# Kernel tuning notes

Measured on AMD Instinct MI355X. Metric: run time of the kernel, lower is better.

The kernel has to match this reference:

```python
import jax, jax.numpy as jnp
import numpy as np

B = 2048
NUM_FIELDS = 32
EMBED = 64
P = NUM_FIELDS * (NUM_FIELDS - 1) // 2  # 496 field pairs

# Pair indices (i < j), identical to the row_idx/col_idx loops in __init__
_ROW, _COL = np.triu_indices(NUM_FIELDS, k=1)
ROW_IDX = jnp.asarray(_ROW, dtype=jnp.int32)
COL_IDX = jnp.asarray(_COL, dtype=jnp.int32)


def setup_inputs() -> dict:
    key = jax.random.key(0)
    k1, k2 = jax.random.split(key)
    emb_inputs = jax.random.normal(k1, (B, NUM_FIELDS, EMBED), dtype=jnp.float32)
    # kernel_type='mat' -> kernel shape (E, P, E), xavier_normal-like init
    fan_in = P * EMBED
    fan_out = EMBED
    std = float(np.sqrt(2.0 / (fan_in + fan_out)))
    kernel = jax.random.normal(k2, (EMBED, P, EMBED), dtype=jnp.float32) * std
    return {"emb_inputs": emb_inputs, "kernel": kernel}


def reference(emb_inputs, kernel):
    # Gather field pairs: p, q shape (B, P, E)
    p = emb_inputs[:, ROW_IDX]
    q = emb_inputs[:, COL_IDX]
    # torch named-tensor chain for kernel_type='mat':
    #   kp[b, h, n] = sum_e p[b, n, e] * kernel[h, n, e]
    #   out[b, n]   = sum_h kp[b, h, n] * q[b, n, h]
    # Fused: out[b, n] = sum_{e, h} p[b, n, e] * kernel[h, n, e] * q[b, n, h]
    return jnp.einsum('bne,hne,bnh->bn', p, kernel, q)
```

## Files before the change

kernel.cpp:

```cpp
#include <hip/hip_runtime.h>


#define B_TOT 2048
#define NF    32
#define EMB   64
#define NP    496
#define BT    64

typedef short bf16x8 __attribute__((ext_vector_type(8)));
typedef short bf16x4 __attribute__((ext_vector_type(4)));
typedef float f32x4  __attribute__((ext_vector_type(4)));
typedef float f32x16 __attribute__((ext_vector_type(16)));

static __device__ inline unsigned f2bf(float f) {
    unsigned u = __builtin_bit_cast(unsigned, f);
    u += 0x7fffu + ((u >> 16) & 1u);
    return u >> 16;
}
static __device__ inline unsigned pack2(float lo, float hi) {
    return f2bf(lo) | (f2bf(hi) << 16);
}
static __device__ inline float bf2f(short s) {
    return __builtin_bit_cast(float, (unsigned)((unsigned short)s) << 16);
}

#define AS1 __attribute__((address_space(1)))
#define AS3 __attribute__((address_space(3)))

__device__ const unsigned char PAIR_T16[120] = {
    0x01,0x02,0x03,0x04,0x05,0x06,0x07,0x08,0x09,0x0A,0x0B,0x0C,0x0D,0x0E,0x0F,
    0x12,0x13,0x14,0x15,0x16,0x17,0x18,0x19,0x1A,0x1B,0x1C,0x1D,0x1E,0x1F,
    0x23,0x24,0x25,0x26,0x27,0x28,0x29,0x2A,0x2B,0x2C,0x2D,0x2E,0x2F,
    0x34,0x35,0x36,0x37,0x38,0x39,0x3A,0x3B,0x3C,0x3D,0x3E,0x3F,
    0x45,0x46,0x47,0x48,0x49,0x4A,0x4B,0x4C,0x4D,0x4E,0x4F,
    0x56,0x57,0x58,0x59,0x5A,0x5B,0x5C,0x5D,0x5E,0x5F,
    0x67,0x68,0x69,0x6A,0x6B,0x6C,0x6D,0x6E,0x6F,
    0x78,0x79,0x7A,0x7B,0x7C,0x7D,0x7E,0x7F,
    0x89,0x8A,0x8B,0x8C,0x8D,0x8E,0x8F,
    0x9A,0x9B,0x9C,0x9D,0x9E,0x9F,
    0xAB,0xAC,0xAD,0xAE,0xAF,
    0xBC,0xBD,0xBE,0xBF,
    0xCD,0xCE,0xCF,
    0xDE,0xDF,
    0xEF
};

__global__ __launch_bounds__(256) void prep(const float* __restrict__ kern,
                                            const float* __restrict__ emb,
                                            short* __restrict__ kb,
                                            short* __restrict__ ebf) {
    __shared__ short w[EMB * 72];
    if (blockIdx.x < NP) {
        const int n = blockIdx.x;
#pragma unroll
        for (int j = 0; j < 4; ++j) {
            const int idx = threadIdx.x + 256 * j;
            const int h = idx >> 4, e4 = idx & 15;
            const f32x4 v = *(const f32x4*)(kern + ((size_t)h * NP + n) * EMB + e4 * 4);
            uint2 u;
            u.x = pack2(v[0], v[1]);
            u.y = pack2(v[2], v[3]);
            *(uint2*)&w[h * 72 + e4 * 4] = u;
        }
        __syncthreads();
#pragma unroll
        for (int j = 0; j < 2; ++j) {
            const int u    = threadIdx.x + 256 * j;
            const int frag = u >> 6, l = u & 63;
            const int h  = (frag >> 2) * 32 + (l & 31);
            const int e0 = (frag & 3) * 16 + (l >> 5) * 8;
            const bf16x8 t = *(const bf16x8*)&w[h * 72 + e0];
            *(bf16x8*)(kb + (size_t)n * 4096 + u * 8) = t;
        }
    } else {
        const int t    = (blockIdx.x - NP) * 256 + threadIdx.x;
        const int cidx = t & 127;
        const int f    = (t >> 7) & 31;
        const int bt16 = t >> 12;
        const int bp = cidx >> 3, x = cidx & 7;
        const int ec = x ^ (bp & 7);
        const float* src = emb + (((size_t)(bt16 * 16 + bp) * NF + f) * EMB + ec * 8);
        const f32x4 a = *(const f32x4*)src;
        const f32x4 b = *(const f32x4*)(src + 4);
        uint4 u;
        u.x = pack2(a[0], a[1]); u.y = pack2(a[2], a[3]);
        u.z = pack2(b[0], b[1]); u.w = pack2(b[2], b[3]);
        *(uint4*)(ebf + (size_t)t * 8) = u;
    }
}

__global__ __launch_bounds__(1024) void opnl_main(
    const short* __restrict__ ebf,
    const short* __restrict__ kb,
    float* __restrict__ out)
{
    __shared__ short elds[64 * 1024];

    const int type = blockIdx.x >> 5;
    const int bt   = blockIdx.x & 31;
    const int b0   = bt * BT;

    int bLo, bHi, npr;
    switch (type) {
        case 0: case 1: bLo = 0;  bHi = 0;  npr = 60; break;
        case 2: case 3: bLo = 16; bHi = 16; npr = 60; break;
        case 4:         bLo = 0;  bHi = 8;  npr = 64; break;
        case 5:         bLo = 8;  bHi = 16; npr = 64; break;
        case 6:         bLo = 0;  bHi = 16; npr = 64; break;
        default:        bLo = 8;  bHi = 8;  npr = 64; break;
    }

    const int lane = threadIdx.x & 63;
    const int wid  = threadIdx.x >> 6;
    const int bp   = lane & 15;
    const int l5   = lane >> 5;
    const int sub_lo = (lane >> 4) & 1;

#pragma unroll
    for (int i = 0; i < 4; ++i) {
        const int s     = wid * 4 + i;
        const int lf    = s >> 2, sub16 = s & 3;
        const int gf    = lf + (lf < 8 ? bLo : bHi);
        const short* src = ebf + ((size_t)((bt * 4 + sub16) * 32 + gf)) * 1024;
        __builtin_amdgcn_global_load_lds((const AS1 void*)(src + lane * 8),
                                         (AS3 void*)&elds[s * 1024], 16, 0, 0);
        __builtin_amdgcn_global_load_lds((const AS1 void*)(src + 512 + lane * 8),
                                         (AS3 void*)&elds[s * 1024 + 512], 16, 0, 0);
    }
    __syncthreads();

    for (int k = 0; k < 4; ++k) {
        int pr = wid + 16 * k;
        if (pr >= npr) pr -= npr;
        int lr, lc;
        if (type < 4) {
            const int pig = __builtin_amdgcn_readfirstlane((type & 1) * 60 + pr);
            const int byt = PAIR_T16[pig];
            lr = byt >> 4; lc = byt & 15;
        } else {
            lr = pr >> 3; lc = 8 + (pr & 7);
        }
        const int R  = lr + (lr < 8 ? bLo : bHi);
        const int C  = lc + (lc < 8 ? bLo : bHi);
        const int nn = R * (63 - R) / 2 + (C - R - 1);

        bf16x8 wf[2][4];
        const bf16x8* wp = (const bf16x8*)(kb + (size_t)nn * 4096);
#pragma unroll
        for (int mt = 0; mt < 2; ++mt)
#pragma unroll
            for (int ks = 0; ks < 4; ++ks)
                wf[mt][ks] = wp[(mt * 4 + ks) * 64 + lane];

#pragma unroll
        for (int hb = 0; hb < 2; ++hb) {
            const int sub16 = hb * 2 + sub_lo;
            const int segp  = (lr * 4 + sub16) * 1024;
            const int segq  = (lc * 4 + sub16) * 1024;

            bf16x8 pf[4];
#pragma unroll
            for (int ks = 0; ks < 4; ++ks) {
                const int ec = ks * 2 + l5;
                pf[ks] = *(const bf16x8*)&elds[segp + (bp * 8 + (ec ^ (bp & 7))) * 8];
            }

            f32x16 acc[2] = {
                f32x16{0,0,0,0,0,0,0,0,0,0,0,0,0,0,0,0},
                f32x16{0,0,0,0,0,0,0,0,0,0,0,0,0,0,0,0}};
#pragma unroll
            for (int ks = 0; ks < 4; ++ks) {
                acc[0] = __builtin_amdgcn_mfma_f32_32x32x16_bf16(
                    wf[0][ks], pf[ks], acc[0], 0, 0, 0);
                acc[1] = __builtin_amdgcn_mfma_f32_32x32x16_bf16(
                    wf[1][ks], pf[ks], acc[1], 0, 0, 0);
            }

            float val = 0.f;
#pragma unroll
            for (int mt = 0; mt < 2; ++mt) {
#pragma unroll
                for (int rg2 = 0; rg2 < 4; ++rg2) {
                    const bf16x4 qv = *(const bf16x4*)
                        &elds[segq + (bp * 8 + ((mt * 4 + rg2) ^ (bp & 7))) * 8 + l5 * 4];
#pragma unroll
                    for (int i = 0; i < 4; ++i)
                        val = fmaf(acc[mt][rg2 * 4 + i], bf2f(qv[i]), val);
                }
            }
            val += __shfl_xor(val, 32, 64);
            if (lane < 32) out[(size_t)(b0 + hb * 32 + lane) * NP + nn] = val;
        }
    }
}

extern "C" void kernel_launch(void* const* d_in, const int* in_sizes, int n_in,
                              void* d_out, int out_size, void* d_ws, size_t ws_size,
                              hipStream_t stream) {
    const float* emb  = (const float*)d_in[0];
    const float* kern = (const float*)d_in[1];
    float*       out  = (float*)d_out;

    short* kb  = (short*)d_ws;
    short* ebf = (short*)((char*)d_ws + (4 << 20));

    prep<<<NP + (B_TOT * NF * EMB / 8) / 256, 256, 0, stream>>>(kern, emb, kb, ebf);
    opnl_main<<<8 * 32, 1024, 0, stream>>>(ebf, kb, out);
}
```

Baseline: 29.31 us.

## Fuse prep and main kernels into one cooperative launch with grid sync

Merges the bf16 conversion/relayout prep kernel and the MFMA main kernel into a single cooperative kernel of 256 blocks that first converts embeddings and kernel weights, then synchronizes the whole grid before computing. It is meant to remove the second kernel launch and the inter-kernel gap. In exchange it pays for a grid-wide barrier, runs the prep phase with only 256 blocks of 1024 threads, and requires all 256 blocks to be co-resident.

```diff
diff --git a/kernel.cpp b/kernel.cpp
--- a/kernel.cpp
+++ b/kernel.cpp
@@ -1,4 +1,7 @@
 #include <hip/hip_runtime.h>
+#include <hip/hip_cooperative_groups.h>
+
+namespace cg = cooperative_groups;
 
 
 #define B_TOT 2048
@@ -45,35 +48,20 @@
     0xEF
 };
 
-__global__ __launch_bounds__(256) void prep(const float* __restrict__ kern,
-                                            const float* __restrict__ emb,
-                                            short* __restrict__ kb,
-                                            short* __restrict__ ebf) {
-    __shared__ short w[EMB * 72];
-    if (blockIdx.x < NP) {
-        const int n = blockIdx.x;
-#pragma unroll
-        for (int j = 0; j < 4; ++j) {
-            const int idx = threadIdx.x + 256 * j;
-            const int h = idx >> 4, e4 = idx & 15;
-            const f32x4 v = *(const f32x4*)(kern + ((size_t)h * NP + n) * EMB + e4 * 4);
-            uint2 u;
-            u.x = pack2(v[0], v[1]);
-            u.y = pack2(v[2], v[3]);
-            *(uint2*)&w[h * 72 + e4 * 4] = u;
-        }
-        __syncthreads();
-#pragma unroll
-        for (int j = 0; j < 2; ++j) {
-            const int u    = threadIdx.x + 256 * j;
-            const int frag = u >> 6, l = u & 63;
-            const int h  = (frag >> 2) * 32 + (l & 31);
-            const int e0 = (frag & 3) * 16 + (l >> 5) * 8;
-            const bf16x8 t = *(const bf16x8*)&w[h * 72 + e0];
-            *(bf16x8*)(kb + (size_t)n * 4096 + u * 8) = t;
-        }
-    } else {
-        const int t    = (blockIdx.x - NP) * 256 + threadIdx.x;
+__global__ __launch_bounds__(1024) void opnl_fused(
+    const float* __restrict__ emb,
+    const float* __restrict__ kern,
+    short* __restrict__ kb,
+    short* __restrict__ ebf,
+    float* __restrict__ out)
+{
+    __shared__ short elds[64 * 1024];
+
+    const int tid = threadIdx.x;
+
+#pragma unroll
+    for (int jt = 0; jt < 2; ++jt) {
+        const int t    = blockIdx.x * 1024 + tid + jt * (256 * 1024);
         const int cidx = t & 127;
         const int f    = (t >> 7) & 31;
         const int bt16 = t >> 12;
@@ -87,14 +75,31 @@
         u.z = pack2(b[0], b[1]); u.w = pack2(b[2], b[3]);
         *(uint4*)(ebf + (size_t)t * 8) = u;
     }
-}
-
-__global__ __launch_bounds__(1024) void opnl_main(
-    const short* __restrict__ ebf,
-    const short* __restrict__ kb,
-    float* __restrict__ out)
-{
-    __shared__ short elds[64 * 1024];
+
+    if (blockIdx.x < 248) {
+#pragma unroll
+        for (int jn = 0; jn < 2; ++jn) {
+            const int n  = blockIdx.x * 2 + jn;
+            const int h  = tid >> 4, e4 = tid & 15;
+            const f32x4 v = *(const f32x4*)(kern + ((size_t)h * NP + n) * EMB + e4 * 4);
+            uint2 u;
+            u.x = pack2(v[0], v[1]);
+            u.y = pack2(v[2], v[3]);
+            *(uint2*)&elds[jn * 4608 + h * 72 + e4 * 4] = u;
+        }
+        __syncthreads();
+        {
+            const int jn = tid >> 9, u = tid & 511;
+            const int n  = blockIdx.x * 2 + jn;
+            const int frag = u >> 6, l = u & 63;
+            const int h  = (frag >> 2) * 32 + (l & 31);
+            const int e0 = (frag & 3) * 16 + (l >> 5) * 8;
+            const bf16x8 t = *(const bf16x8*)&elds[jn * 4608 + h * 72 + e0];
+            *(bf16x8*)(kb + (size_t)n * 4096 + u * 8) = t;
+        }
+    }
+
+    cg::this_grid().sync();
 
     const int type = blockIdx.x >> 5;
     const int bt   = blockIdx.x & 31;
@@ -110,8 +115,8 @@
         default:        bLo = 8;  bHi = 8;  npr = 64; break;
     }
 
-    const int lane = threadIdx.x & 63;
-    const int wid  = threadIdx.x >> 6;
+    const int lane = tid & 63;
+    const int wid  = tid >> 6;
     const int bp   = lane & 15;
     const int l5   = lane >> 5;
     const int sub_lo = (lane >> 4) & 1;
@@ -204,6 +209,7 @@
     short* kb  = (short*)d_ws;
     short* ebf = (short*)((char*)d_ws + (4 << 20));
 
-    prep<<<NP + (B_TOT * NF * EMB / 8) / 256, 256, 0, stream>>>(kern, emb, kb, ebf);
-    opnl_main<<<8 * 32, 1024, 0, stream>>>(ebf, kb, out);
-}
+    void* args[] = {(void*)&emb, (void*)&kern, (void*)&kb, (void*)&ebf, (void*)&out};
+    hipLaunchCooperativeKernel((void*)opnl_fused, dim3(256), dim3(1024),
+                               args, 0, stream);
+}
```

New measurement: 76.67 us. +161.6%, slower.

## Fuse embedding bf16 conversion into main kernel, drop intermediate buffer

Applied to the files above, without the earlier changes.

The prep kernel no longer converts embeddings to a swizzled bf16 workspace buffer. The main kernel now reads fp32 embeddings directly from global memory, converts them to bf16 in registers and writes them into the swizzled LDS layout. Block index mapping also changes to interleave the eight pair types within each batch tile, which may improve L2 reuse of the embedding rows. This removes a global write and re-read of the bf16 embedding copy, but each main block now reads twice as many bytes (fp32) and does conversion work before the barrier. Embedding rows are also re-read from global by all eight type blocks.

```diff
diff --git a/kernel.cpp b/kernel.cpp
--- a/kernel.cpp
+++ b/kernel.cpp
@@ -23,9 +23,6 @@
 static __device__ inline float bf2f(short s) {
     return __builtin_bit_cast(float, (unsigned)((unsigned short)s) << 16);
 }
-
-#define AS1 __attribute__((address_space(1)))
-#define AS3 __attribute__((address_space(3)))
 
 __device__ const unsigned char PAIR_T16[120] = {
     0x01,0x02,0x03,0x04,0x05,0x06,0x07,0x08,0x09,0x0A,0x0B,0x0C,0x0D,0x0E,0x0F,
@@ -45,59 +42,41 @@
     0xEF
 };
 
-__global__ __launch_bounds__(256) void prep(const float* __restrict__ kern,
-                                            const float* __restrict__ emb,
-                                            short* __restrict__ kb,
-                                            short* __restrict__ ebf) {
+__global__ __launch_bounds__(256) void prep_kern(const float* __restrict__ kern,
+                                                 short* __restrict__ kb) {
+    const int n = blockIdx.x;
     __shared__ short w[EMB * 72];
-    if (blockIdx.x < NP) {
-        const int n = blockIdx.x;
-#pragma unroll
-        for (int j = 0; j < 4; ++j) {
-            const int idx = threadIdx.x + 256 * j;
-            const int h = idx >> 4, e4 = idx & 15;
-            const f32x4 v = *(const f32x4*)(kern + ((size_t)h * NP + n) * EMB + e4 * 4);
-            uint2 u;
-            u.x = pack2(v[0], v[1]);
-            u.y = pack2(v[2], v[3]);
-            *(uint2*)&w[h * 72 + e4 * 4] = u;
-        }
-        __syncthreads();
-#pragma unroll
-        for (int j = 0; j < 2; ++j) {
-            const int u    = threadIdx.x + 256 * j;
-            const int frag = u >> 6, l = u & 63;
-            const int h  = (frag >> 2) * 32 + (l & 31);
-            const int e0 = (frag & 3) * 16 + (l >> 5) * 8;
-            const bf16x8 t = *(const bf16x8*)&w[h * 72 + e0];
-            *(bf16x8*)(kb + (size_t)n * 4096 + u * 8) = t;
-        }
-    } else {
-        const int t    = (blockIdx.x - NP) * 256 + threadIdx.x;
-        const int cidx = t & 127;
-        const int f    = (t >> 7) & 31;
-        const int bt16 = t >> 12;
-        const int bp = cidx >> 3, x = cidx & 7;
-        const int ec = x ^ (bp & 7);
-        const float* src = emb + (((size_t)(bt16 * 16 + bp) * NF + f) * EMB + ec * 8);
-        const f32x4 a = *(const f32x4*)src;
-        const f32x4 b = *(const f32x4*)(src + 4);
-        uint4 u;
-        u.x = pack2(a[0], a[1]); u.y = pack2(a[2], a[3]);
-        u.z = pack2(b[0], b[1]); u.w = pack2(b[2], b[3]);
-        *(uint4*)(ebf + (size_t)t * 8) = u;
+#pragma unroll
+    for (int j = 0; j < 4; ++j) {
+        const int idx = threadIdx.x + 256 * j;
+        const int h = idx >> 4, e4 = idx & 15;
+        const f32x4 v = *(const f32x4*)(kern + ((size_t)h * NP + n) * EMB + e4 * 4);
+        uint2 u;
+        u.x = pack2(v[0], v[1]);
+        u.y = pack2(v[2], v[3]);
+        *(uint2*)&w[h * 72 + e4 * 4] = u;
+    }
+    __syncthreads();
+#pragma unroll
+    for (int j = 0; j < 2; ++j) {
+        const int u    = threadIdx.x + 256 * j;
+        const int frag = u >> 6, l = u & 63;
+        const int h  = (frag >> 2) * 32 + (l & 31);
+        const int e0 = (frag & 3) * 16 + (l >> 5) * 8;
+        const bf16x8 t = *(const bf16x8*)&w[h * 72 + e0];
+        *(bf16x8*)(kb + (size_t)n * 4096 + u * 8) = t;
     }
 }
 
 __global__ __launch_bounds__(1024) void opnl_main(
-    const short* __restrict__ ebf,
+    const float* __restrict__ emb,
     const short* __restrict__ kb,
     float* __restrict__ out)
 {
     __shared__ short elds[64 * 1024];
 
-    const int type = blockIdx.x >> 5;
-    const int bt   = blockIdx.x & 31;
+    const int type = blockIdx.x & 7;
+    const int bt   = blockIdx.x >> 3;
     const int b0   = bt * BT;
 
     int bLo, bHi, npr;
@@ -110,22 +89,42 @@
         default:        bLo = 8;  bHi = 8;  npr = 64; break;
     }
 
-    const int lane = threadIdx.x & 63;
-    const int wid  = threadIdx.x >> 6;
+    const int tid  = threadIdx.x;
+    const int lane = tid & 63;
+    const int wid  = tid >> 6;
     const int bp   = lane & 15;
     const int l5   = lane >> 5;
     const int sub_lo = (lane >> 4) & 1;
 
-#pragma unroll
-    for (int i = 0; i < 4; ++i) {
-        const int s     = wid * 4 + i;
-        const int lf    = s >> 2, sub16 = s & 3;
-        const int gf    = lf + (lf < 8 ? bLo : bHi);
-        const short* src = ebf + ((size_t)((bt * 4 + sub16) * 32 + gf)) * 1024;
-        __builtin_amdgcn_global_load_lds((const AS1 void*)(src + lane * 8),
-                                         (AS3 void*)&elds[s * 1024], 16, 0, 0);
-        __builtin_amdgcn_global_load_lds((const AS1 void*)(src + 512 + lane * 8),
-                                         (AS3 void*)&elds[s * 1024 + 512], 16, 0, 0);
+    {
+        const int run = tid >> 3, j = tid & 7;
+        const int bl  = run >> 1, o = run & 1;
+        const int sub16 = bl >> 4, sbp = bl & 15;
+        const int gf0 = o ? (bHi + 8) : bLo;
+        const float* src = emb + ((size_t)(b0 + bl) * NF + gf0) * EMB;
+
+        f32x4 v[4][4];
+#pragma unroll
+        for (int s = 0; s < 4; ++s)
+#pragma unroll
+            for (int k = 0; k < 4; ++k)
+                v[s][k] = *(const f32x4*)(src + s * 128 + k * 32 + j * 4);
+
+#pragma unroll
+        for (int s = 0; s < 4; ++s)
+#pragma unroll
+            for (int k = 0; k < 4; ++k) {
+                const int fi   = 2 * s + (k >> 1);
+                const int lf   = o ? 8 + fi : fi;
+                const int seg  = lf * 4 + sub16;
+                const int ec   = (k & 1) * 4 + (j >> 1);
+                const int half = j & 1;
+                const int c    = sbp * 8 + (ec ^ (sbp & 7));
+                uint2 u;
+                u.x = pack2(v[s][k][0], v[s][k][1]);
+                u.y = pack2(v[s][k][2], v[s][k][3]);
+                *(uint2*)&elds[seg * 1024 + c * 8 + half * 4] = u;
+            }
     }
     __syncthreads();
 
@@ -200,10 +199,8 @@
     const float* emb  = (const float*)d_in[0];
     const float* kern = (const float*)d_in[1];
     float*       out  = (float*)d_out;
-
-    short* kb  = (short*)d_ws;
-    short* ebf = (short*)((char*)d_ws + (4 << 20));
-
-    prep<<<NP + (B_TOT * NF * EMB / 8) / 256, 256, 0, stream>>>(kern, emb, kb, ebf);
-    opnl_main<<<8 * 32, 1024, 0, stream>>>(ebf, kb, out);
-}
+    short*       kb   = (short*)d_ws;
+
+    prep_kern<<<NP, 256, 0, stream>>>(kern, kb);
+    opnl_main<<<8 * 32, 1024, 0, stream>>>(emb, kb, out);
+}
```

New measurement: 36.41 us. 1.24x slower.
